# Kernel tuning notes

Measured on AMD Instinct MI355X. Metric: run time of the kernel, lower is better.

Reference implementation:

```python
import jax, jax.numpy as jnp
import numpy as np

UNITS = 512
D_Q = 1024
D_V = 1024


def setup_inputs() -> dict:
    key = jax.random.key(0)
    ks = jax.random.split(key, 12)
    B, L = 32, 2048
    inp = {
        "query": jax.random.normal(ks[0], (B, D_Q), jnp.float32),
        "values": jax.random.normal(ks[1], (B, L, D_V), jnp.float32),
        "mask": jnp.zeros((B, L, 1), jnp.float32),
        "previous_scores": jax.random.uniform(ks[2], (B, L, 1), jnp.float32),
        "timestep": 3,
        # Dense params (glorot-ish scale)
        "Wh": jax.random.normal(ks[3], (D_Q, UNITS), jnp.float32) / np.sqrt(D_Q),
        "bh": jnp.zeros((UNITS,), jnp.float32),
        "Wv": jax.random.normal(ks[4], (D_V, UNITS), jnp.float32) / np.sqrt(D_V),
        "bv": jnp.zeros((UNITS,), jnp.float32),
        "Wp": jax.random.normal(ks[5], (3, UNITS), jnp.float32) / np.sqrt(3.0),
        "bp": jnp.zeros((UNITS,), jnp.float32),
        "Wm": jax.random.normal(ks[6], (5, UNITS), jnp.float32) / np.sqrt(5.0),
        "bm": jnp.zeros((UNITS,), jnp.float32),
        "vw": jax.random.normal(ks[7], (UNITS, 1), jnp.float32) / np.sqrt(UNITS),
        "vb": jnp.zeros((1,), jnp.float32),
    }
    return inp


def reference(query, values, mask, previous_scores, timestep,
              Wh, bh, Wv, bv, Wp, bp, Wm, bm, vw, vb):
    B, L, _ = mask.shape
    # input_lengths: 1 + count of mask==0 along seq, tiled across L  -> [B, L, 1]
    input_len = 1.0 + jnp.sum((mask == 0).astype(jnp.float32), axis=1)  # [B, 1]
    input_len = jnp.broadcast_to(input_len, (B, L))[..., None]          # [B, L, 1]
    # positional features: [1+timestep, 2+pos, input_len], logged -> [B, L, 3]
    pos2 = jnp.stack([jnp.full((L,), 1.0 + timestep, jnp.float32),
                      2.0 + jnp.arange(L, dtype=jnp.float32)], axis=-1)  # [L, 2]
    pos2 = jnp.broadcast_to(pos2[None], (B, L, 2))
    positional = jnp.log(jnp.concatenate([pos2, input_len], axis=-1))    # [B, L, 3]
    # markov: sliding window of width 5 over zero-padded previous scores -> [B, L, 5]
    padded = jnp.pad(previous_scores[:, :, 0], ((0, 0), (2, 2)))         # [B, L+4]
    widx = jnp.arange(L)[:, None] + jnp.arange(5)[None, :]               # [L, 5]
    markov = padded[:, widx]                                             # [B, L, 5]
    # additive attention score
    summand = (jnp.einsum('bq,qu->bu', query, Wh) + bh)[:, None, :]      # [B, 1, U]
    summand = summand + (jnp.einsum('blv,vu->blu', values, Wv) + bv)
    summand = summand + (jnp.einsum('blp,pu->blu', positional, Wp) + bp)
    summand = summand + (jnp.einsum('blm,mu->blu', markov, Wm) + bm)
    score = jnp.einsum('blu,uo->blo', jnp.tanh(summand), vw) + vb        # [B, L, 1]
    score = score + mask * (-1e9)
    attention_weights = jax.nn.softmax(score, axis=1)                    # [B, L, 1]
    context_vector = jnp.sum(attention_weights * values, axis=1)         # [B, D_V]
    return (context_vector, attention_weights)
```

## Files before the change

### kernel.cpp

```cpp
#include <hip/hip_runtime.h>
#include <hip/hip_bf16.h>
#include <math.h>

#define NB 32
#define LL 2048
#define DV 1024
#define NU 512
#define NM (NB * LL)

typedef __attribute__((ext_vector_type(8))) short short8;
typedef __attribute__((ext_vector_type(4))) float f32x4;

#define GLL16(g, l)                                                            \
  __builtin_amdgcn_global_load_lds(                                            \
      (const __attribute__((address_space(1))) void*)(g),                      \
      (__attribute__((address_space(3))) void*)(l), 16, 0, 0)

__device__ __forceinline__ float fast_tanh(float x) {
  x = fminf(fmaxf(x, -15.f), 15.f);
  float e = __expf(2.f * x);
  return (e - 1.f) / (e + 1.f);
}

__global__ __launch_bounds__(256) void masksum_kernel(
    const float* __restrict__ mask, float* __restrict__ loglen) {
  int b = blockIdx.x, tid = threadIdx.x;
  int lane = tid & 63, wid = tid >> 6;
  float c = 0.f;
#pragma unroll
  for (int j = 0; j < 8; j++)
    c += (mask[(size_t)b * LL + j * 256 + tid] == 0.f) ? 1.f : 0.f;
#pragma unroll
  for (int o = 32; o >= 1; o >>= 1) c += __shfl_xor(c, o, 64);
  __shared__ float red[4];
  if (lane == 0) red[wid] = c;
  __syncthreads();
  if (tid == 0) loglen[b] = logf(1.f + red[0] + red[1] + red[2] + red[3]);
}

__global__ __launch_bounds__(256) void wvpack_kernel(
    const float* __restrict__ Wv, __hip_bfloat16* __restrict__ wvpk) {
  int t = blockIdx.x * 256 + threadIdx.x;
  int u4 = t & 127;
  int kg = t >> 7;
  int k0 = kg * 8;
  int kt = kg >> 2;
  int q = kg & 3;
  float4 f[8];
#pragma unroll
  for (int j = 0; j < 8; j++)
    f[j] = *(const float4*)(Wv + (size_t)(k0 + j) * NU + u4 * 4);
#pragma unroll
  for (int e = 0; e < 4; e++) {
    int u = u4 * 4 + e;
    int nt = u >> 8, n = u & 255;
    int c = q ^ ((n >> 1) & 3);
    int idx = nt * 32768 + kt * 1024 + n * 4 + c;
    const float* fe = (const float*)&f[0] + e;
    union {
      __hip_bfloat162 h2[4];
      int4 v;
    } pk;
#pragma unroll
    for (int m = 0; m < 4; m++)
      pk.h2[m] = __float22bfloat162_rn(make_float2(fe[(2 * m) * 4], fe[(2 * m + 1) * 4]));
    ((int4*)wvpk)[idx] = pk.v;
  }
}

__global__ __launch_bounds__(256) void h_kernel(
    const float* __restrict__ q, const float* __restrict__ Wh,
    const float* __restrict__ bh, const float* __restrict__ bv,
    const float* __restrict__ bp, const float* __restrict__ bm,
    const float* __restrict__ Wp, const int* __restrict__ ts,
    const float* __restrict__ loglen, float* __restrict__ h) {
  int u0 = blockIdx.x * 64;
  int bq = blockIdx.y;
  int tid = threadIdx.x;
  int u = tid & 63, bsub = tid >> 6;
  int b0 = bq * 8 + bsub * 2, b1 = b0 + 1;

  __shared__ float qsL[8][1024];
#pragma unroll
  for (int j = 0; j < 8; j++) {
    int f = j * 256 + tid;
    int bl = f >> 8, k4 = f & 255;
    *(float4*)&qsL[bl][k4 * 4] =
        *(const float4*)(q + (size_t)(bq * 8 + bl) * 1024 + k4 * 4);
  }
  __syncthreads();

  float a0e = 0.f, a0o = 0.f, a1e = 0.f, a1o = 0.f;
#pragma unroll 16
  for (int k = 0; k < 1024; k += 2) {
    float w0 = Wh[(size_t)k * NU + u0 + u];
    float w1 = Wh[(size_t)(k + 1) * NU + u0 + u];
    a0e += w0 * qsL[bsub * 2][k];
    a1e += w0 * qsL[bsub * 2 + 1][k];
    a0o += w1 * qsL[bsub * 2][k + 1];
    a1o += w1 * qsL[bsub * 2 + 1][k + 1];
  }
  float acc0 = a0e + a0o, acc1 = a1e + a1o;

  int uu = u0 + u;
  float lt = logf(1.0f + (float)ts[0]);
  float bias = bh[uu] + bv[uu] + bp[uu] + bm[uu] + lt * Wp[uu];
  float wp2 = Wp[2 * NU + uu];
  h[b0 * NU + uu] = acc0 + bias + loglen[b0] * wp2;
  h[b1 * NU + uu] = acc1 + bias + loglen[b1] * wp2;
}

__global__ __launch_bounds__(256, 2) void score_kernel(
    const float* __restrict__ values, const __hip_bfloat16* __restrict__ wvpk,
    const float* __restrict__ h, const float* __restrict__ Wp,
    const float* __restrict__ Wm, const float* __restrict__ vw,
    const float* __restrict__ prev, float* __restrict__ partial) {
  int lin = blockIdx.x;
  int group = lin >> 4, sub = lin & 15;
  int ntile = sub >> 3;
  int mtile = group * 8 + (sub & 7);
  int tid = threadIdx.x;
  int lane = tid & 63, wid = tid >> 6;
  int wr = wid >> 1, wc = wid & 1;
  int col = lane & 15, quad = lane >> 4;
  int b = mtile >> 4;
  int l0 = (mtile & 15) << 7;
  int rowbase = mtile << 7;

  __shared__ __align__(16) char AsB[2][8192];
  __shared__ __align__(16) char BsB[2][16384];
  __shared__ float hL[256], wp1L[256], vwL[256], wmL[5][256];
  __shared__ float loglS[128], prevs[132], scoreAcc[128];

  {
    int u = ntile * 256 + tid;
    hL[tid] = h[b * NU + u];
    wp1L[tid] = Wp[NU + u];
    vwL[tid] = vw[u];
#pragma unroll
    for (int j = 0; j < 5; j++) wmL[j][tid] = Wm[j * NU + u];
  }
  if (tid < 128) {
    loglS[tid] = __logf(2.0f + (float)(l0 + tid));
    scoreAcc[tid] = 0.f;
  }
  if (tid < 132) {
    int li = l0 - 2 + tid;
    prevs[tid] = (li >= 0 && li < LL) ? prev[(size_t)b * LL + li] : 0.f;
  }

  f32x4 acc[4][8];
  f32x4 zero4 = {0.f, 0.f, 0.f, 0.f};
#pragma unroll
  for (int i = 0; i < 4; i++)
#pragma unroll
    for (int j = 0; j < 8; j++) acc[i][j] = zero4;

  int row = tid >> 1, h0 = tid & 1;
  const float* abase = values + (size_t)(rowbase + row) * DV + h0 * 16;
  int s_sw = (row >> 1) & 3;
  int aoff0 = row * 64 + (((h0 * 2) ^ s_sw) * 16);
  int aoff1 = row * 64 + (((h0 * 2 + 1) ^ s_sw) * 16);
  const char* bbase = (const char*)wvpk + (size_t)ntile * 32 * 16384;
  int boff = tid * 16;

  float4 preA[2][4];

  {
#pragma unroll
    for (int d = 0; d < 2; d++) {
      const float4* p = (const float4*)(abase + d * 32);
#pragma unroll
      for (int j = 0; j < 4; j++) preA[d][j] = p[j];
    }
    GLL16(bbase + boff, BsB[0] + boff);
    GLL16(bbase + boff + 4096, BsB[0] + boff + 4096);
    GLL16(bbase + boff + 8192, BsB[0] + boff + 8192);
    GLL16(bbase + boff + 12288, BsB[0] + boff + 12288);
    float4 f0 = preA[0][0], f1 = preA[0][1];
    float4 f2 = preA[0][2], f3 = preA[0][3];
    union {
      __hip_bfloat162 h2[8];
      int4 qq[2];
    } pk;
    pk.h2[0] = __float22bfloat162_rn(make_float2(f0.x, f0.y));
    pk.h2[1] = __float22bfloat162_rn(make_float2(f0.z, f0.w));
    pk.h2[2] = __float22bfloat162_rn(make_float2(f1.x, f1.y));
    pk.h2[3] = __float22bfloat162_rn(make_float2(f1.z, f1.w));
    pk.h2[4] = __float22bfloat162_rn(make_float2(f2.x, f2.y));
    pk.h2[5] = __float22bfloat162_rn(make_float2(f2.z, f2.w));
    pk.h2[6] = __float22bfloat162_rn(make_float2(f3.x, f3.y));
    pk.h2[7] = __float22bfloat162_rn(make_float2(f3.z, f3.w));
    *(int4*)(AsB[0] + aoff0) = pk.qq[0];
    *(int4*)(AsB[0] + aoff1) = pk.qq[1];
    const float4* nx = (const float4*)(abase + 2 * 32);
    preA[0][0] = nx[0];
    preA[0][1] = nx[1];
    preA[0][2] = nx[2];
    preA[0][3] = nx[3];
    __syncthreads();
  }

#define KSTEP(KT, CBUF, OSLOT, DO_STAGE, DO_RELOAD)                            \
  {                                                                            \
    if (DO_STAGE) {                                                            \
      const char* bsrc = bbase + (size_t)((KT) + 1) * 16384;                   \
      GLL16(bsrc + boff, BsB[(CBUF) ^ 1] + boff);                              \
      GLL16(bsrc + boff + 4096, BsB[(CBUF) ^ 1] + boff + 4096);                \
      GLL16(bsrc + boff + 8192, BsB[(CBUF) ^ 1] + boff + 8192);                \
      GLL16(bsrc + boff + 12288, BsB[(CBUF) ^ 1] + boff + 12288);              \
      float4 f0 = preA[OSLOT][0], f1 = preA[OSLOT][1];                         \
      float4 f2 = preA[OSLOT][2], f3 = preA[OSLOT][3];                         \
      union {                                                                  \
        __hip_bfloat162 h2[8];                                                 \
        int4 qq[2];                                                            \
      } pk;                                                                    \
      pk.h2[0] = __float22bfloat162_rn(make_float2(f0.x, f0.y));               \
      pk.h2[1] = __float22bfloat162_rn(make_float2(f0.z, f0.w));               \
      pk.h2[2] = __float22bfloat162_rn(make_float2(f1.x, f1.y));               \
      pk.h2[3] = __float22bfloat162_rn(make_float2(f1.z, f1.w));               \
      pk.h2[4] = __float22bfloat162_rn(make_float2(f2.x, f2.y));               \
      pk.h2[5] = __float22bfloat162_rn(make_float2(f2.z, f2.w));               \
      pk.h2[6] = __float22bfloat162_rn(make_float2(f3.x, f3.y));               \
      pk.h2[7] = __float22bfloat162_rn(make_float2(f3.z, f3.w));               \
      *(int4*)(AsB[(CBUF) ^ 1] + aoff0) = pk.qq[0];                            \
      *(int4*)(AsB[(CBUF) ^ 1] + aoff1) = pk.qq[1];                            \
      if (DO_RELOAD) {                                                         \
        const float4* nx = (const float4*)(abase + ((KT) + 3) * 32);           \
        preA[OSLOT][0] = nx[0];                                                \
        preA[OSLOT][1] = nx[1];                                                \
        preA[OSLOT][2] = nx[2];                                                \
        preA[OSLOT][3] = nx[3];                                                \
      }                                                                        \
    }                                                                          \
    short8 aF[4];                                                              \
    _Pragma("unroll") for (int t = 0; t < 4; t++) {                            \
      int m = wr * 64 + t * 16 + col;                                          \
      aF[t] = *(const short8*)(AsB[CBUF] + m * 64 +                            \
                               ((quad ^ ((m >> 1) & 3)) * 16));                \
    }                                                                          \
    _Pragma("unroll") for (int tc = 0; tc < 8; tc++) {                         \
      int n = wc * 128 + tc * 16 + col;                                        \
      short8 bF =                                                              \
          *(const short8*)(BsB[CBUF] + n * 64 + ((quad ^ ((n >> 1) & 3)) * 16)); \
      _Pragma("unroll") for (int tr = 0; tr < 4; tr++) acc[tr][tc] =           \
          __builtin_amdgcn_mfma_f32_16x16x32_bf16(aF[tr], bF, acc[tr][tc], 0,  \
                                                  0, 0);                       \
    }                                                                          \
    __syncthreads();                                                           \
  }

  for (int kto = 0; kto < 14; kto++) {
    KSTEP(2 * kto, 0, 1, 1, 1);
    KSTEP(2 * kto + 1, 1, 0, 1, 1);
  }
  KSTEP(28, 0, 1, 1, 1);
  KSTEP(29, 1, 0, 1, 0);
  KSTEP(30, 0, 1, 1, 0);
  KSTEP(31, 1, 0, 0, 0);
#undef KSTEP

  int rb = wr * 64;
#pragma unroll
  for (int tr = 0; tr < 4; tr++) {
    float ps[4] = {0.f, 0.f, 0.f, 0.f};
#pragma unroll
    for (int tc = 0; tc < 8; tc++) {
      int uc = wc * 128 + tc * 16 + col;
      float hh = hL[uc], wp1 = wp1L[uc], vv = vwL[uc];
      float m0 = wmL[0][uc], m1 = wmL[1][uc], m2 = wmL[2][uc],
            m3 = wmL[3][uc], m4 = wmL[4][uc];
      int r0 = rb + tr * 16 + quad * 4;
#pragma unroll
      for (int i = 0; i < 4; i++) {
        int r = r0 + i;
        float e = hh + loglS[r] * wp1 + prevs[r] * m0 + prevs[r + 1] * m1 +
                  prevs[r + 2] * m2 + prevs[r + 3] * m3 + prevs[r + 4] * m4;
        float sv = acc[tr][tc][i] + e;
        ps[i] += fast_tanh(sv) * vv;
      }
    }
#pragma unroll
    for (int i = 0; i < 4; i++) {
      float v = ps[i];
      v += __shfl_xor(v, 1, 64);
      v += __shfl_xor(v, 2, 64);
      v += __shfl_xor(v, 4, 64);
      v += __shfl_xor(v, 8, 64);
      if (col == 0) atomicAdd(&scoreAcc[rb + tr * 16 + quad * 4 + i], v);
    }
  }
  __syncthreads();
  if (tid < 128)
    partial[(size_t)ntile * NM + rowbase + tid] = scoreAcc[tid];
}

__global__ __launch_bounds__(256) void softmax_kernel(
    const float* __restrict__ partial, const float* __restrict__ mask,
    float* __restrict__ aw) {
  int b = blockIdx.x, tid = threadIdx.x;
  int lane = tid & 63, wid = tid >> 6;
  __shared__ float redmax[4], redsum[4];
  float sc[8];
  float mx = -3.0e38f;
#pragma unroll
  for (int j = 0; j < 8; j++) {
    size_t base = (size_t)b * LL + j * 256 + tid;
    float s = partial[base] + partial[(size_t)NM + base];
    s += mask[base] * -1.0e9f;
    sc[j] = s;
    mx = fmaxf(mx, s);
  }
#pragma unroll
  for (int o = 32; o >= 1; o >>= 1) mx = fmaxf(mx, __shfl_xor(mx, o, 64));
  if (lane == 0) redmax[wid] = mx;
  __syncthreads();
  mx = fmaxf(fmaxf(redmax[0], redmax[1]), fmaxf(redmax[2], redmax[3]));
  float sum = 0.f;
#pragma unroll
  for (int j = 0; j < 8; j++) {
    float e = __expf(sc[j] - mx);
    sc[j] = e;
    sum += e;
  }
#pragma unroll
  for (int o = 32; o >= 1; o >>= 1) sum += __shfl_xor(sum, o, 64);
  if (lane == 0) redsum[wid] = sum;
  __syncthreads();
  sum = redsum[0] + redsum[1] + redsum[2] + redsum[3];
  float inv = 1.0f / sum;
#pragma unroll
  for (int j = 0; j < 8; j++)
    aw[(size_t)b * LL + j * 256 + tid] = sc[j] * inv;
}

__global__ __launch_bounds__(1024) void ctx_kernel(
    const float* __restrict__ values, const float* __restrict__ aw,
    float* __restrict__ out) {
  int b = blockIdx.x >> 1, half = blockIdx.x & 1;
  int tid = threadIdx.x;
  int s = tid & 255, rg = tid >> 8;
  int l0 = half * 1024;

  __shared__ float awL[1024];
  __shared__ f32x4 red[4][256];

  awL[tid] = aw[(size_t)b * LL + l0 + tid];
  __syncthreads();

  const float4* vbase =
      (const float4*)(values + ((size_t)b * LL + l0 + rg * 256) * DV) + s;
  const float* awr = awL + rg * 256;
  float4 acc = make_float4(0.f, 0.f, 0.f, 0.f);
  for (int i0 = 0; i0 < 256; i0 += 8) {
    float4 v[8];
#pragma unroll
    for (int j = 0; j < 8; j++) v[j] = vbase[(size_t)(i0 + j) * 256];
#pragma unroll
    for (int j = 0; j < 8; j++) {
      float w = awr[i0 + j];
      acc.x += w * v[j].x;
      acc.y += w * v[j].y;
      acc.z += w * v[j].z;
      acc.w += w * v[j].w;
    }
  }
  f32x4 a4 = {acc.x, acc.y, acc.z, acc.w};
  red[rg][s] = a4;
  __syncthreads();
  if (tid < 256) {
    f32x4 r = red[0][s];
    f32x4 r1 = red[1][s], r2 = red[2][s], r3 = red[3][s];
    r += r1;
    r += r2;
    r += r3;
    float* o = out + (size_t)b * DV + s * 4;
    atomicAdd(o + 0, r[0]);
    atomicAdd(o + 1, r[1]);
    atomicAdd(o + 2, r[2]);
    atomicAdd(o + 3, r[3]);
  }
}

extern "C" void kernel_launch(void* const* d_in, const int* in_sizes, int n_in,
                              void* d_out, int out_size, void* d_ws,
                              size_t ws_size, hipStream_t stream) {
  const float* query = (const float*)d_in[0];
  const float* values = (const float*)d_in[1];
  const float* mask = (const float*)d_in[2];
  const float* prev = (const float*)d_in[3];
  const int* ts = (const int*)d_in[4];
  const float* Wh = (const float*)d_in[5];
  const float* bh = (const float*)d_in[6];
  const float* Wv = (const float*)d_in[7];
  const float* bv = (const float*)d_in[8];
  const float* Wp = (const float*)d_in[9];
  const float* bp = (const float*)d_in[10];
  const float* Wm = (const float*)d_in[11];
  const float* bm = (const float*)d_in[12];
  const float* vw = (const float*)d_in[13];

  float* out = (float*)d_out;
  float* ws = (float*)d_ws;
  float* loglen = ws;
  float* h = ws + 1024;
  float* partial = ws + 32768;
  __hip_bfloat16* wvpk =
      (__hip_bfloat16*)((char*)d_ws + (size_t)163840 * 4);
  float* aw = out + 32768;

  hipMemsetAsync(d_out, 0, 32768 * sizeof(float), stream);
  masksum_kernel<<<NB, 256, 0, stream>>>(mask, loglen);
  wvpack_kernel<<<64, 256, 0, stream>>>(Wv, wvpk);
  h_kernel<<<dim3(8, 4), 256, 0, stream>>>(query, Wh, bh, bv, bp, bm, Wp, ts,
                                           loglen, h);
  score_kernel<<<1024, 256, 0, stream>>>(values, wvpk, h, Wp, Wm, vw, prev,
                                         partial);
  softmax_kernel<<<NB, 256, 0, stream>>>(partial, mask, aw);
  ctx_kernel<<<64, 1024, 0, stream>>>(values, aw, out);
}
```

Baseline: 543.3 us.

## Use 512-thread score blocks with smaller per-wave tiles; split ctx over more blocks

The score GEMM kernel now runs 8 waves per block instead of 4. Each wave covers a 64x64 output tile instead of 64x128, which halves its accumulator registers and its per-thread staging loads, and the launch bound now targets 4 blocks per CU. The context kernel is split into 8 sequence chunks per batch instead of 2, giving 256 blocks so more CUs stream the values tensor. This trades extra atomic or partial reduction traffic and more waves competing for LDS for higher occupancy and better latency hiding.

```diff
diff --git a/kernel.cpp b/kernel.cpp
--- a/kernel.cpp
+++ b/kernel.cpp
@@ -110,7 +110,7 @@
   h[b1 * NU + uu] = acc1 + bias + loglen[b1] * wp2;
 }
 
-__global__ __launch_bounds__(256, 2) void score_kernel(
+__global__ __launch_bounds__(512, 4) void score_kernel(
     const float* __restrict__ values, const __hip_bfloat16* __restrict__ wvpk,
     const float* __restrict__ h, const float* __restrict__ Wp,
     const float* __restrict__ Wm, const float* __restrict__ vw,
@@ -121,7 +121,7 @@
   int mtile = group * 8 + (sub & 7);
   int tid = threadIdx.x;
   int lane = tid & 63, wid = tid >> 6;
-  int wr = wid >> 1, wc = wid & 1;
+  int wr = wid >> 2, wc = wid & 3;
   int col = lane & 15, quad = lane >> 4;
   int b = mtile >> 4;
   int l0 = (mtile & 15) << 7;
@@ -132,7 +132,7 @@
   __shared__ float hL[256], wp1L[256], vwL[256], wmL[5][256];
   __shared__ float loglS[128], prevs[132], scoreAcc[128];
 
-  {
+  if (tid < 256) {
     int u = ntile * 256 + tid;
     hL[tid] = h[b * NU + u];
     wp1L[tid] = Wp[NU + u];
@@ -149,55 +149,47 @@
     prevs[tid] = (li >= 0 && li < LL) ? prev[(size_t)b * LL + li] : 0.f;
   }
 
-  f32x4 acc[4][8];
+  f32x4 acc[4][4];
   f32x4 zero4 = {0.f, 0.f, 0.f, 0.f};
 #pragma unroll
   for (int i = 0; i < 4; i++)
 #pragma unroll
-    for (int j = 0; j < 8; j++) acc[i][j] = zero4;
-
-  int row = tid >> 1, h0 = tid & 1;
-  const float* abase = values + (size_t)(rowbase + row) * DV + h0 * 16;
+    for (int j = 0; j < 4; j++) acc[i][j] = zero4;
+
+  int row = tid >> 2, h0 = tid & 3;
+  const float* abase = values + (size_t)(rowbase + row) * DV + h0 * 8;
   int s_sw = (row >> 1) & 3;
-  int aoff0 = row * 64 + (((h0 * 2) ^ s_sw) * 16);
-  int aoff1 = row * 64 + (((h0 * 2 + 1) ^ s_sw) * 16);
+  int aoff = row * 64 + ((h0 ^ s_sw) * 16);
   const char* bbase = (const char*)wvpk + (size_t)ntile * 32 * 16384;
   int boff = tid * 16;
 
-  float4 preA[2][4];
+  float4 preA[2][2];
+
+#define CVT_STORE(SLOT, DSTBUF)                                                \
+  {                                                                            \
+    float4 f0 = preA[SLOT][0], f1 = preA[SLOT][1];                             \
+    union {                                                                    \
+      __hip_bfloat162 h2[4];                                                   \
+      int4 v;                                                                  \
+    } pk;                                                                      \
+    pk.h2[0] = __float22bfloat162_rn(make_float2(f0.x, f0.y));                 \
+    pk.h2[1] = __float22bfloat162_rn(make_float2(f0.z, f0.w));                 \
+    pk.h2[2] = __float22bfloat162_rn(make_float2(f1.x, f1.y));                 \
+    pk.h2[3] = __float22bfloat162_rn(make_float2(f1.z, f1.w));                 \
+    *(int4*)(AsB[DSTBUF] + aoff) = pk.v;                                       \
+  }
 
   {
 #pragma unroll
     for (int d = 0; d < 2; d++) {
-      const float4* p = (const float4*)(abase + d * 32);
-#pragma unroll
-      for (int j = 0; j < 4; j++) preA[d][j] = p[j];
+      preA[d][0] = *(const float4*)(abase + d * 32);
+      preA[d][1] = *(const float4*)(abase + d * 32 + 4);
     }
     GLL16(bbase + boff, BsB[0] + boff);
-    GLL16(bbase + boff + 4096, BsB[0] + boff + 4096);
     GLL16(bbase + boff + 8192, BsB[0] + boff + 8192);
-    GLL16(bbase + boff + 12288, BsB[0] + boff + 12288);
-    float4 f0 = preA[0][0], f1 = preA[0][1];
-    float4 f2 = preA[0][2], f3 = preA[0][3];
-    union {
-      __hip_bfloat162 h2[8];
-      int4 qq[2];
-    } pk;
-    pk.h2[0] = __float22bfloat162_rn(make_float2(f0.x, f0.y));
-    pk.h2[1] = __float22bfloat162_rn(make_float2(f0.z, f0.w));
-    pk.h2[2] = __float22bfloat162_rn(make_float2(f1.x, f1.y));
-    pk.h2[3] = __float22bfloat162_rn(make_float2(f1.z, f1.w));
-    pk.h2[4] = __float22bfloat162_rn(make_float2(f2.x, f2.y));
-    pk.h2[5] = __float22bfloat162_rn(make_float2(f2.z, f2.w));
-    pk.h2[6] = __float22bfloat162_rn(make_float2(f3.x, f3.y));
-    pk.h2[7] = __float22bfloat162_rn(make_float2(f3.z, f3.w));
-    *(int4*)(AsB[0] + aoff0) = pk.qq[0];
-    *(int4*)(AsB[0] + aoff1) = pk.qq[1];
-    const float4* nx = (const float4*)(abase + 2 * 32);
-    preA[0][0] = nx[0];
-    preA[0][1] = nx[1];
-    preA[0][2] = nx[2];
-    preA[0][3] = nx[3];
+    CVT_STORE(0, 0);
+    preA[0][0] = *(const float4*)(abase + 2 * 32);
+    preA[0][1] = *(const float4*)(abase + 2 * 32 + 4);
     __syncthreads();
   }
 
@@ -206,31 +198,11 @@
     if (DO_STAGE) {                                                            \
       const char* bsrc = bbase + (size_t)((KT) + 1) * 16384;                   \
       GLL16(bsrc + boff, BsB[(CBUF) ^ 1] + boff);                              \
-      GLL16(bsrc + boff + 4096, BsB[(CBUF) ^ 1] + boff + 4096);                \
       GLL16(bsrc + boff + 8192, BsB[(CBUF) ^ 1] + boff + 8192);                \
-      GLL16(bsrc + boff + 12288, BsB[(CBUF) ^ 1] + boff + 12288);              \
-      float4 f0 = preA[OSLOT][0], f1 = preA[OSLOT][1];                         \
-      float4 f2 = preA[OSLOT][2], f3 = preA[OSLOT][3];                         \
-      union {                                                                  \
-        __hip_bfloat162 h2[8];                                                 \
-        int4 qq[2];                                                            \
-      } pk;                                                                    \
-      pk.h2[0] = __float22bfloat162_rn(make_float2(f0.x, f0.y));               \
-      pk.h2[1] = __float22bfloat162_rn(make_float2(f0.z, f0.w));               \
-      pk.h2[2] = __float22bfloat162_rn(make_float2(f1.x, f1.y));               \
-      pk.h2[3] = __float22bfloat162_rn(make_float2(f1.z, f1.w));               \
-      pk.h2[4] = __float22bfloat162_rn(make_float2(f2.x, f2.y));               \
-      pk.h2[5] = __float22bfloat162_rn(make_float2(f2.z, f2.w));               \
-      pk.h2[6] = __float22bfloat162_rn(make_float2(f3.x, f3.y));               \
-      pk.h2[7] = __float22bfloat162_rn(make_float2(f3.z, f3.w));               \
-      *(int4*)(AsB[(CBUF) ^ 1] + aoff0) = pk.qq[0];                            \
-      *(int4*)(AsB[(CBUF) ^ 1] + aoff1) = pk.qq[1];                            \
+      CVT_STORE(OSLOT, (CBUF) ^ 1);                                            \
       if (DO_RELOAD) {                                                         \
-        const float4* nx = (const float4*)(abase + ((KT) + 3) * 32);           \
-        preA[OSLOT][0] = nx[0];                                                \
-        preA[OSLOT][1] = nx[1];                                                \
-        preA[OSLOT][2] = nx[2];                                                \
-        preA[OSLOT][3] = nx[3];                                                \
+        preA[OSLOT][0] = *(const float4*)(abase + ((KT) + 3) * 32);            \
+        preA[OSLOT][1] = *(const float4*)(abase + ((KT) + 3) * 32 + 4);        \
       }                                                                        \
     }                                                                          \
     short8 aF[4];                                                              \
@@ -239,8 +211,8 @@
       aF[t] = *(const short8*)(AsB[CBUF] + m * 64 +                            \
                                ((quad ^ ((m >> 1) & 3)) * 16));                \
     }                                                                          \
-    _Pragma("unroll") for (int tc = 0; tc < 8; tc++) {                         \
-      int n = wc * 128 + tc * 16 + col;                                        \
+    _Pragma("unroll") for (int tc = 0; tc < 4; tc++) {                         \
+      int n = wc * 64 + tc * 16 + col;                                         \
       short8 bF =                                                              \
           *(const short8*)(BsB[CBUF] + n * 64 + ((quad ^ ((n >> 1) & 3)) * 16)); \
       _Pragma("unroll") for (int tr = 0; tr < 4; tr++) acc[tr][tc] =           \
@@ -259,14 +231,15 @@
   KSTEP(30, 0, 1, 1, 0);
   KSTEP(31, 1, 0, 0, 0);
 #undef KSTEP
+#undef CVT_STORE
 
   int rb = wr * 64;
 #pragma unroll
   for (int tr = 0; tr < 4; tr++) {
     float ps[4] = {0.f, 0.f, 0.f, 0.f};
 #pragma unroll
-    for (int tc = 0; tc < 8; tc++) {
-      int uc = wc * 128 + tc * 16 + col;
+    for (int tc = 0; tc < 4; tc++) {
+      int uc = wc * 64 + tc * 16 + col;
       float hh = hL[uc], wp1 = wp1L[uc], vv = vwL[uc];
       float m0 = wmL[0][uc], m1 = wmL[1][uc], m2 = wmL[2][uc],
             m3 = wmL[3][uc], m4 = wmL[4][uc];
@@ -337,22 +310,22 @@
 __global__ __launch_bounds__(1024) void ctx_kernel(
     const float* __restrict__ values, const float* __restrict__ aw,
     float* __restrict__ out) {
-  int b = blockIdx.x >> 1, half = blockIdx.x & 1;
+  int b = blockIdx.x >> 3, chunk = blockIdx.x & 7;
   int tid = threadIdx.x;
   int s = tid & 255, rg = tid >> 8;
-  int l0 = half * 1024;
-
-  __shared__ float awL[1024];
+  int l0 = chunk * 256;
+
+  __shared__ float awL[256];
   __shared__ f32x4 red[4][256];
 
-  awL[tid] = aw[(size_t)b * LL + l0 + tid];
+  if (tid < 256) awL[tid] = aw[(size_t)b * LL + l0 + tid];
   __syncthreads();
 
   const float4* vbase =
-      (const float4*)(values + ((size_t)b * LL + l0 + rg * 256) * DV) + s;
-  const float* awr = awL + rg * 256;
+      (const float4*)(values + ((size_t)b * LL + l0 + rg * 64) * DV) + s;
+  const float* awr = awL + rg * 64;
   float4 acc = make_float4(0.f, 0.f, 0.f, 0.f);
-  for (int i0 = 0; i0 < 256; i0 += 8) {
+  for (int i0 = 0; i0 < 64; i0 += 8) {
     float4 v[8];
 #pragma unroll
     for (int j = 0; j < 8; j++) v[j] = vbase[(size_t)(i0 + j) * 256];
@@ -414,8 +387,8 @@
   wvpack_kernel<<<64, 256, 0, stream>>>(Wv, wvpk);
   h_kernel<<<dim3(8, 4), 256, 0, stream>>>(query, Wh, bh, bv, bp, bm, Wp, ts,
                                            loglen, h);
-  score_kernel<<<1024, 256, 0, stream>>>(values, wvpk, h, Wp, Wm, vw, prev,
+  score_kernel<<<1024, 512, 0, stream>>>(values, wvpk, h, Wp, Wm, vw, prev,
                                          partial);
   softmax_kernel<<<NB, 256, 0, stream>>>(partial, mask, aw);
-  ctx_kernel<<<64, 1024, 0, stream>>>(values, aw, out);
-}
+  ctx_kernel<<<256, 1024, 0, stream>>>(values, aw, out);
+}
```

Result: faster. 524.1 us (-3.5%).
